# Optimization experiments

Hardware: AMD Instinct MI355X
Metric: run time of the kernel (lower is better)

Reference implementation:

```python
import jax, jax.numpy as jnp
import numpy as np
import math

FACTOR = 1  # init kwarg

def setup_inputs() -> dict:
    key = jax.random.key(0)
    k1, k2 = jax.random.split(key)
    B, H, C, L = 32, 8, 64, 1024
    values = jax.random.normal(k1, (B, H, C, L), dtype=jnp.float32)
    corr = jax.random.uniform(k2, (B, H, C, L), dtype=jnp.float32)
    return {"values": values, "corr": corr}

def reference(values, corr):
    # Faithful translation of Auto_attn.time_delay_training.
    B, H, C, L = values.shape
    top_k = int(FACTOR * math.log(L))  # static: depends only on L
    # mean over head then channel -> [B, L]
    mean_value = corr.mean(axis=(1, 2))
    # top-k delays shared across the batch (argmax of batch-mean correlation)
    _, index = jax.lax.top_k(mean_value.mean(axis=0), top_k)  # [top_k]
    # per-batch weights at the selected delays -> [B, top_k]
    weights = mean_value[:, index]
    tmp_corr = jax.nn.softmax(weights, axis=-1)  # [B, top_k]
    # roll(values, -index[i], axis=-1) == gather at (t + index[i]) mod L
    gather_idx = (jnp.arange(L)[None, :] + index[:, None]) % L  # [top_k, L]
    pattern = jnp.take(values, gather_idx, axis=-1)  # [B, H, C, top_k, L]
    # softmax-weighted aggregation over the top_k delays
    delays_agg = jnp.einsum('bhckl,bk->bhcl', pattern, tmp_corr)
    return delays_agg
```

## Files before the change

kernel.cpp:

```cpp
#include <hip/hip_runtime.h>
#include <math.h>

#define B 32
#define H 8
#define C 64
#define L 1024
#define HC (H * C)
#define K 6

#define SLICES 8
#define SLICE_L (L / SLICES)
#define GROUPS 8
#define ROWS_PER_GROUP (HC / GROUPS)

__global__ __launch_bounds__(256) void mean_value_kernel(
    const float* __restrict__ corr, float* __restrict__ mean_value) {
    __shared__ float sacc[GROUPS * SLICE_L];
    int blk = blockIdx.x;
    int b = blk / SLICES;
    int s = blk % SLICES;
    int t = threadIdx.x;
    int g = t >> 5;
    int j = t & 31;

    const float4* base =
        (const float4*)(corr + (size_t)b * HC * L + s * SLICE_L);
    float4 acc = make_float4(0.f, 0.f, 0.f, 0.f);
    #pragma unroll 8
    for (int i = 0; i < ROWS_PER_GROUP; ++i) {
        int r = g + GROUPS * i;
        float4 v = base[(size_t)r * (L / 4) + j];
        acc.x += v.x; acc.y += v.y; acc.z += v.z; acc.w += v.w;
    }
    ((float4*)sacc)[g * (SLICE_L / 4) + j] = acc;
    __syncthreads();

    if (t < SLICE_L) {
        float m = 0.f;
        #pragma unroll
        for (int g2 = 0; g2 < GROUPS; ++g2) m += sacc[g2 * SLICE_L + t];
        mean_value[b * L + s * SLICE_L + t] = m * (1.0f / HC);
    }
}

__global__ __launch_bounds__(1024) void topk_softmax_kernel(
    const float* __restrict__ mean_value,
    float* __restrict__ tmp_corr,
    int* __restrict__ index_out) {
    __shared__ float wval[16];
    __shared__ int   widx[16];
    __shared__ int   sel[K];
    int t = threadIdx.x;
    int lane = t & 63;
    int wave = t >> 6;

    float s = 0.f;
    for (int b = 0; b < B; ++b) s += mean_value[b * L + t];
    float cm = s * (1.0f / B);
    int   ci = t;

    for (int k = 0; k < K; ++k) {
        float v = cm; int i = ci;
        #pragma unroll
        for (int off = 32; off >= 1; off >>= 1) {
            float v2 = __shfl_xor(v, off, 64);
            int   i2 = __shfl_xor(i, off, 64);
            if (v2 > v || (v2 == v && i2 < i)) { v = v2; i = i2; }
        }
        if (lane == 0) { wval[wave] = v; widx[wave] = i; }
        __syncthreads();
        if (wave == 0) {
            float v3 = (lane < 16) ? wval[lane] : -3.0e38f;
            int   i3 = (lane < 16) ? widx[lane] : 0x7fffffff;
            #pragma unroll
            for (int off = 8; off >= 1; off >>= 1) {
                float v2 = __shfl_xor(v3, off, 64);
                int   i2 = __shfl_xor(i3, off, 64);
                if (v2 > v3 || (v2 == v3 && i2 < i3)) { v3 = v2; i3 = i2; }
            }
            if (lane == 0) sel[k] = i3;
        }
        __syncthreads();
        if (ci == sel[k]) cm = -3.0e38f;
    }

    if (t < K) index_out[t] = sel[t];
    if (t < B) {
        float w[K];
        float m = -3.0e38f;
        for (int k = 0; k < K; ++k) {
            w[k] = mean_value[t * L + sel[k]];
            m = fmaxf(m, w[k]);
        }
        float sum = 0.f;
        for (int k = 0; k < K; ++k) { w[k] = expf(w[k] - m); sum += w[k]; }
        float inv = 1.0f / sum;
        for (int k = 0; k < K; ++k) tmp_corr[t * K + k] = w[k] * inv;
    }
}

__global__ __launch_bounds__(256) void agg_kernel(
    const float* __restrict__ values,
    const float* __restrict__ tmp_corr,
    const int* __restrict__ index,
    float* __restrict__ out) {
    __shared__ float row[L];
    __shared__ float ws[K];
    __shared__ int   is[K];
    int blk = blockIdx.x;
    int b = blk / HC;
    int tid = threadIdx.x;

    ((float4*)row)[tid] = ((const float4*)(values + (size_t)blk * L))[tid];
    if (tid < K) { ws[tid] = tmp_corr[b * K + tid]; is[tid] = index[tid]; }
    __syncthreads();

    float w[K]; int d[K];
    #pragma unroll
    for (int k = 0; k < K; ++k) { w[k] = ws[k]; d[k] = is[k]; }

    float* orow = out + (size_t)blk * L;
    #pragma unroll
    for (int off = 0; off < L; off += 256) {
        int l = tid + off;
        float acc = 0.f;
        #pragma unroll
        for (int k = 0; k < K; ++k)
            acc += w[k] * row[(l + d[k]) & (L - 1)];
        orow[l] = acc;
    }
}

extern "C" void kernel_launch(void* const* d_in, const int* in_sizes, int n_in,
                              void* d_out, int out_size, void* d_ws, size_t ws_size,
                              hipStream_t stream) {
    const float* values = (const float*)d_in[0];
    const float* corr   = (const float*)d_in[1];
    float* out = (float*)d_out;

    float* mean_value = (float*)d_ws;
    float* tmp_corr   = mean_value + (size_t)B * L;
    int*   index      = (int*)(tmp_corr + B * K);

    mean_value_kernel<<<B * SLICES, 256, 0, stream>>>(corr, mean_value);
    topk_softmax_kernel<<<1, 1024, 0, stream>>>(mean_value, tmp_corr, index);
    agg_kernel<<<B * H * C, 256, 0, stream>>>(values, tmp_corr, index, out);
}
```

Measured before the change: 178.0 us.

## Fuse top-k selection into mean kernel via last-block atomic counter

Merges the mean-reduction and top-k/softmax kernels into one launch, where the last block to finish (tracked by an atomic counter plus thread fences) does the column mean, top-k and softmax using 256 threads with 4 elements each. It also doubles the slice and group counts so the mean reduction launches twice as many blocks. This removes one kernel launch and its gap, but adds a memset launch, and the top-k now runs on 256 threads instead of 1024.

```diff
diff --git a/kernel.cpp b/kernel.cpp
--- a/kernel.cpp
+++ b/kernel.cpp
@@ -8,20 +8,26 @@
 #define HC (H * C)
 #define K 6
 
-#define SLICES 8
+#define SLICES 16
 #define SLICE_L (L / SLICES)
-#define GROUPS 8
+#define GROUPS 16
 #define ROWS_PER_GROUP (HC / GROUPS)
+#define TOTAL_BLOCKS (B * SLICES)
 
-__global__ __launch_bounds__(256) void mean_value_kernel(
-    const float* __restrict__ corr, float* __restrict__ mean_value) {
+__global__ __launch_bounds__(256) void mean_topk_kernel(
+    const float* __restrict__ corr,
+    float* __restrict__ mean_value,
+    float* __restrict__ tmp_corr,
+    int* __restrict__ index_out,
+    unsigned int* __restrict__ counter) {
     __shared__ float sacc[GROUPS * SLICE_L];
+    __shared__ unsigned int s_old;
     int blk = blockIdx.x;
     int b = blk / SLICES;
     int s = blk % SLICES;
     int t = threadIdx.x;
-    int g = t >> 5;
-    int j = t & 31;
+    int g = t >> 4;
+    int j = t & 15;
 
     const float4* base =
         (const float4*)(corr + (size_t)b * HC * L + s * SLICE_L);
@@ -41,39 +47,47 @@
         for (int g2 = 0; g2 < GROUPS; ++g2) m += sacc[g2 * SLICE_L + t];
         mean_value[b * L + s * SLICE_L + t] = m * (1.0f / HC);
     }
-}
 
-__global__ __launch_bounds__(1024) void topk_softmax_kernel(
-    const float* __restrict__ mean_value,
-    float* __restrict__ tmp_corr,
-    int* __restrict__ index_out) {
-    __shared__ float wval[16];
-    __shared__ int   widx[16];
+    __threadfence();
+    if (t == 0) s_old = atomicAdd(counter, 1u);
+    __syncthreads();
+    if (s_old != TOTAL_BLOCKS - 1) return;
+    __threadfence();
+
+    float cm[4];
+    #pragma unroll
+    for (int q = 0; q < 4; ++q) {
+        int l = t + 256 * q;
+        float sum = 0.f;
+        #pragma unroll
+        for (int bb = 0; bb < B; ++bb) sum += mean_value[bb * L + l];
+        cm[q] = sum * (1.0f / B);
+    }
+
+    __shared__ float wv[4];
+    __shared__ int   wi[4];
     __shared__ int   sel[K];
-    int t = threadIdx.x;
     int lane = t & 63;
     int wave = t >> 6;
 
-    float s = 0.f;
-    for (int b = 0; b < B; ++b) s += mean_value[b * L + t];
-    float cm = s * (1.0f / B);
-    int   ci = t;
-
     for (int k = 0; k < K; ++k) {
-        float v = cm; int i = ci;
+        float v = -3.0e38f; int i = 0x7fffffff;
+        #pragma unroll
+        for (int q = 0; q < 4; ++q)
+            if (cm[q] > v) { v = cm[q]; i = t + 256 * q; }
         #pragma unroll
         for (int off = 32; off >= 1; off >>= 1) {
             float v2 = __shfl_xor(v, off, 64);
             int   i2 = __shfl_xor(i, off, 64);
             if (v2 > v || (v2 == v && i2 < i)) { v = v2; i = i2; }
         }
-        if (lane == 0) { wval[wave] = v; widx[wave] = i; }
+        if (lane == 0) { wv[wave] = v; wi[wave] = i; }
         __syncthreads();
         if (wave == 0) {
-            float v3 = (lane < 16) ? wval[lane] : -3.0e38f;
-            int   i3 = (lane < 16) ? widx[lane] : 0x7fffffff;
+            float v3 = (lane < 4) ? wv[lane] : -3.0e38f;
+            int   i3 = (lane < 4) ? wi[lane] : 0x7fffffff;
             #pragma unroll
-            for (int off = 8; off >= 1; off >>= 1) {
+            for (int off = 2; off >= 1; off >>= 1) {
                 float v2 = __shfl_xor(v3, off, 64);
                 int   i2 = __shfl_xor(i3, off, 64);
                 if (v2 > v3 || (v2 == v3 && i2 < i3)) { v3 = v2; i3 = i2; }
@@ -81,20 +95,25 @@
             if (lane == 0) sel[k] = i3;
         }
         __syncthreads();
-        if (ci == sel[k]) cm = -3.0e38f;
+        #pragma unroll
+        for (int q = 0; q < 4; ++q)
+            if (t + 256 * q == sel[k]) cm[q] = -3.0e38f;
     }
 
     if (t < K) index_out[t] = sel[t];
     if (t < B) {
         float w[K];
         float m = -3.0e38f;
+        #pragma unroll
         for (int k = 0; k < K; ++k) {
             w[k] = mean_value[t * L + sel[k]];
             m = fmaxf(m, w[k]);
         }
         float sum = 0.f;
+        #pragma unroll
         for (int k = 0; k < K; ++k) { w[k] = expf(w[k] - m); sum += w[k]; }
         float inv = 1.0f / sum;
+        #pragma unroll
         for (int k = 0; k < K; ++k) tmp_corr[t * K + k] = w[k] * inv;
     }
 }
@@ -141,8 +160,10 @@
     float* mean_value = (float*)d_ws;
     float* tmp_corr   = mean_value + (size_t)B * L;
     int*   index      = (int*)(tmp_corr + B * K);
+    unsigned int* counter = (unsigned int*)(index + K + 2);
 
-    mean_value_kernel<<<B * SLICES, 256, 0, stream>>>(corr, mean_value);
-    topk_softmax_kernel<<<1, 1024, 0, stream>>>(mean_value, tmp_corr, index);
+    hipMemsetAsync(counter, 0, sizeof(unsigned int), stream);
+    mean_topk_kernel<<<TOTAL_BLOCKS, 256, 0, stream>>>(
+        corr, mean_value, tmp_corr, index, counter);
     agg_kernel<<<B * H * C, 256, 0, stream>>>(values, tmp_corr, index, out);
 }
```

After: 223.5 us. 1.26x slower.
